# Kernel tuning notes

Hardware: AMD Instinct MI355X
Metric: run time of the kernel (lower is better)

The kernel has to match this reference:

```python
import jax, jax.numpy as jnp
import numpy as np

N, K, D, H = 20000, 32, 256, 8
HD = D // H
DFF = 4 * D
EPS = 1e-5


def _layernorm(x, gamma, beta):
    mu = jnp.mean(x, axis=-1, keepdims=True)
    var = jnp.mean(jnp.square(x - mu), axis=-1, keepdims=True)
    return (x - mu) * jax.lax.rsqrt(var + EPS) * gamma + beta


def setup_inputs() -> dict:
    key = jax.random.key(0)
    ks = jax.random.split(key, 16)
    s = 0.02
    return {
        "x": jax.random.normal(ks[0], (N, D), jnp.float32),
        "attention_samples": jax.random.randint(ks[1], (N, K), 0, N),
        "Wq": jax.random.normal(ks[2], (D, D), jnp.float32) * s,
        "bq": jnp.zeros((D,), jnp.float32),
        "Wk": jax.random.normal(ks[3], (D, D), jnp.float32) * s,
        "bk": jnp.zeros((D,), jnp.float32),
        "Wv": jax.random.normal(ks[4], (D, D), jnp.float32) * s,
        "bv": jnp.zeros((D,), jnp.float32),
        "Wo": jax.random.normal(ks[5], (D, D), jnp.float32) * s,
        "bo": jnp.zeros((D,), jnp.float32),
        "W1": jax.random.normal(ks[6], (D, DFF), jnp.float32) * s,
        "b1": jnp.zeros((DFF,), jnp.float32),
        "W2": jax.random.normal(ks[7], (DFF, D), jnp.float32) * s,
        "b2": jnp.zeros((D,), jnp.float32),
        "g1": jnp.ones((D,), jnp.float32),
        "be1": jnp.zeros((D,), jnp.float32),
        "g2": jnp.ones((D,), jnp.float32),
        "be2": jnp.zeros((D,), jnp.float32),
    }


def reference(x, attention_samples, Wq, bq, Wk, bk, Wv, bv, Wo, bo,
              W1, b1, W2, b2, g1, be1, g2, be2):
    # --- per-node MHA: query = node itself, keys/values = k sampled neighbors ---
    q = (x @ Wq + bq).reshape(N, H, HD)                    # [N,H,hd]
    g = x[attention_samples]                               # [N,K,D] gathered neighbors
    kk = (g @ Wk + bk).reshape(N, K, H, HD)                # [N,K,H,hd]
    vv = (g @ Wv + bv).reshape(N, K, H, HD)
    scale = 1.0 / jnp.sqrt(jnp.asarray(HD, x.dtype))
    scores = jnp.einsum("nhd,nkhd->nhk", q, kk) * scale    # [N,H,K]
    attn = jax.nn.softmax(scores, axis=-1)
    o = jnp.einsum("nhk,nkhd->nhd", attn, vv).reshape(N, D)
    attn_out = o @ Wo + bo                                 # out_proj
    x = _layernorm(x + attn_out, g1, be1)
    # --- FFN ---
    ff = jax.nn.relu(x @ W1 + b1) @ W2 + b2
    x = _layernorm(x + ff, g2, be2)
    return x
```

## Files before the change

### kernel.cpp

```cpp
#include <hip/hip_runtime.h>

#define NN 20000
#define KNEI 32
#define DIM 256
#define NHEAD 8
#define HDIM 32
#define DFFN 1024
#define QKVD 768

typedef __attribute__((ext_vector_type(8))) __bf16 bf16x8;
typedef __attribute__((ext_vector_type(8))) unsigned short u16x8;
typedef __attribute__((ext_vector_type(4))) unsigned short u16x4;
typedef __attribute__((ext_vector_type(4))) float f32x4;
typedef __attribute__((ext_vector_type(2))) float f32x2;

static __device__ __forceinline__ float b2f(unsigned short u) {
    return __builtin_bit_cast(float, (unsigned)u << 16);
}
static __device__ __forceinline__ float blo(unsigned w) {
    return __builtin_bit_cast(float, w << 16);
}
static __device__ __forceinline__ float bhi(unsigned w) {
    return __builtin_bit_cast(float, w & 0xffff0000u);
}
static __device__ __forceinline__ unsigned short f2b(float f) {
    unsigned u = __builtin_bit_cast(unsigned, f);
    return (unsigned short)((u + 0x7fff + ((u >> 16) & 1)) >> 16);
}

static __device__ __forceinline__ unsigned char fp8enc(float v) {
#if defined(__HIP_DEVICE_COMPILE__) && __has_builtin(__builtin_amdgcn_cvt_pk_fp8_f32)
    return (unsigned char)(__builtin_amdgcn_cvt_pk_fp8_f32(v, v, 0u, false) & 0xffu);
#else
    unsigned u = __builtin_bit_cast(unsigned, v);
    unsigned s = u >> 31;
    unsigned a = u & 0x7fffffffu;
    if (a >= 0x43e00000u) return (unsigned char)((s << 7) | 0x7e);
    float af = __builtin_bit_cast(float, a);
    if (af < 0.015625f) {
        unsigned r = (unsigned)(af * 512.0f + 0.5f);
        if (r >= 8u) return (unsigned char)((s << 7) | 0x08);
        return (unsigned char)((s << 7) | r);
    }
    unsigned lsb = (a >> 20) & 1u;
    a += 0x7ffffu + lsb;
    unsigned e = (a >> 23) - 120u;
    unsigned m = (a >> 20) & 7u;
    unsigned code = (e << 3) | m;
    if (code > 0x7eu) code = 0x7eu;
    return (unsigned char)((s << 7) | code);
#endif
}

template<int SEL>
static __device__ __forceinline__ float fp8dec(unsigned word) {
#if defined(__HIP_DEVICE_COMPILE__) && __has_builtin(__builtin_amdgcn_cvt_f32_fp8)
    return __builtin_amdgcn_cvt_f32_fp8(word, SEL);
#else
    unsigned b = (word >> (SEL * 8)) & 0xffu;
    unsigned s = (b >> 7) & 1u;
    unsigned e = (b >> 3) & 0xfu;
    unsigned m = b & 7u;
    float v;
    if (e == 0) v = (float)m * 0.001953125f;
    else        v = __builtin_bit_cast(float, ((e + 120u) << 23) | (m << 20));
    return s ? -v : v;
#endif
}

template<bool HI>
static __device__ __forceinline__ f32x2 fp8pk(unsigned word) {
#if defined(__HIP_DEVICE_COMPILE__) && __has_builtin(__builtin_amdgcn_cvt_pk_f32_fp8)
    return __builtin_amdgcn_cvt_pk_f32_fp8((int)word, HI);
#else
    f32x2 r;
    r.x = fp8dec<HI ? 2 : 0>(word);
    r.y = fp8dec<HI ? 3 : 1>(word);
    return r;
#endif
}

#define GLD16(src, dst)                                                          \
    __builtin_amdgcn_global_load_lds(                                            \
        (const __attribute__((address_space(1))) void*)(const void*)(src),       \
        (__attribute__((address_space(3))) void*)(void*)(dst), 16, 0, 0)

template<int BM, int RELU, int WF32, int WBF16, int SPLIT>
__global__ __launch_bounds__(256) void gemm_mfma(const unsigned short* __restrict__ A,
                                                 const unsigned short* __restrict__ Bt,
                                                 const float* __restrict__ bias,
                                                 float* __restrict__ Cf,
                                                 unsigned short* __restrict__ Cb,
                                                 unsigned char* __restrict__ kvp,
                                                 int M, int N, int K)
{
    constexpr int BN = 128, BK = 32;
    constexpr int MI = BM / 32;
    constexpr int NI = BN / 32;

    __shared__ unsigned short As[BM * BK];
    __shared__ unsigned short Bs[BN * BK];

    const int tid  = threadIdx.x;
    const int wid  = tid >> 6;
    const int lane = tid & 63;
    const int bm = blockIdx.x * BM;
    const int bn = blockIdx.y * BN;
    const int wr = (wid >> 1) * (BM / 2);
    const int wc = (wid & 1) * (BN / 2);
    const int r0   = lane & 15;
    const int kblk = (lane >> 4) * 8;

    f32x4 acc[MI][NI];
    #pragma unroll
    for (int i = 0; i < MI; ++i)
        #pragma unroll
        for (int j = 0; j < NI; ++j)
            acc[i][j] = (f32x4){0.f, 0.f, 0.f, 0.f};

    for (int k0 = 0; k0 < K; k0 += BK) {
        #pragma unroll
        for (int t = 0; t < (BM * 4) / 256; ++t) {
            int c = t * 256 + tid;
            int row = bm + (c >> 2);
            if (row >= M) row = M - 1;
            GLD16(A + (size_t)row * K + k0 + (c & 3) * 8,
                  &As[(t * 256 + wid * 64) * 8]);
        }
        #pragma unroll
        for (int t = 0; t < (BN * 4) / 256; ++t) {
            int c = t * 256 + tid;
            GLD16(Bt + (size_t)(bn + (c >> 2)) * K + k0 + (c & 3) * 8,
                  &Bs[(t * 256 + wid * 64) * 8]);
        }
        __syncthreads();

        bf16x8 af[MI], bfr[NI];
        #pragma unroll
        for (int mi = 0; mi < MI; ++mi)
            af[mi] = __builtin_bit_cast(bf16x8,
                     *(const u16x8*)&As[(wr + mi * 16 + r0) * BK + kblk]);
        #pragma unroll
        for (int ni = 0; ni < NI; ++ni)
            bfr[ni] = __builtin_bit_cast(bf16x8,
                     *(const u16x8*)&Bs[(wc + ni * 16 + r0) * BK + kblk]);
        #pragma unroll
        for (int mi = 0; mi < MI; ++mi)
            #pragma unroll
            for (int ni = 0; ni < NI; ++ni)
                acc[mi][ni] = __builtin_amdgcn_mfma_f32_16x16x32_bf16(
                    af[mi], bfr[ni], acc[mi][ni], 0, 0, 0);
        __syncthreads();
    }

    const int r4 = (lane >> 4) * 4;
    #pragma unroll
    for (int mi = 0; mi < MI; ++mi)
        #pragma unroll
        for (int ni = 0; ni < NI; ++ni) {
            const int col = bn + wc + ni * 16 + r0;
            const float bb = bias[col];
            #pragma unroll
            for (int r = 0; r < 4; ++r) {
                const int row = bm + wr + mi * 16 + r4 + r;
                if (row < M) {
                    float v = acc[mi][ni][r] + bb;
                    if (RELU) v = fmaxf(v, 0.f);
                    if (SPLIT) {
                        if (col < 256) {
                            Cb[(size_t)row * DIM + col] = f2b(v);
                        } else {
                            const int cc  = col - 256;
                            const int isV = cc >> 8;
                            const int hh  = (cc & 255) >> 5;
                            const int dd  = cc & 31;
                            kvp[((size_t)(hh >> 1) * NN + row) * 128
                                + isV * 64 + (hh & 1) * 32 + dd] = fp8enc(v);
                        }
                    } else {
                        if (WF32)  Cf[(size_t)row * N + col] = v;
                        if (WBF16) Cb[(size_t)row * N + col] = f2b(v);
                    }
                }
            }
        }
}

__global__ __launch_bounds__(256) void attn_f8(const unsigned short* __restrict__ q,
                                               const unsigned char* __restrict__ kvp,
                                               const int* __restrict__ samp,
                                               unsigned short* __restrict__ o)
{
    __shared__ int pkbuf[4][128];

    const int bid = blockIdx.x;
    const int hp  = bid & 3;
    const int tid = threadIdx.x;
    const int wid = tid >> 6;
    const int n   = (bid >> 2) * 4 + wid;
    const int lane = tid & 63;
    const int j = lane & 31;
    const int hs = lane >> 5;
    const int h = hp * 2 + hs;

    const int kidx = samp[n * KNEI + j];

    const uint4* qp = (const uint4*)(q + (size_t)n * DIM + h * HDIM);
    const uint4 qa = qp[0], qb = qp[1], qc = qp[2], qd = qp[3];
    const unsigned qw[16] = {qa.x, qa.y, qa.z, qa.w, qb.x, qb.y, qb.z, qb.w,
                             qc.x, qc.y, qc.z, qc.w, qd.x, qd.y, qd.z, qd.w};

    const unsigned char* krow = kvp + ((size_t)hp * NN + kidx) * 128 + hs * 32;
    const uint4 k0 = *(const uint4*)krow;
    const uint4 k1 = *(const uint4*)(krow + 16);
    const unsigned kw[8] = {k0.x, k0.y, k0.z, k0.w, k1.x, k1.y, k1.z, k1.w};

    float s = 0.f;
    #pragma unroll
    for (int i = 0; i < 8; ++i) {
        f32x2 ka = fp8pk<false>(kw[i]);
        f32x2 kb = fp8pk<true>(kw[i]);
        unsigned q0 = qw[2 * i], q1 = qw[2 * i + 1];
        s = fmaf(blo(q0), ka.x, s);
        s = fmaf(bhi(q0), ka.y, s);
        s = fmaf(blo(q1), kb.x, s);
        s = fmaf(bhi(q1), kb.y, s);
    }
    s *= 0.17677669529663687f;

    float m = s;
    #pragma unroll
    for (int sh = 16; sh; sh >>= 1) m = fmaxf(m, __shfl_xor(m, sh));
    float e = __expf(s - m);
    float sum = e;
    #pragma unroll
    for (int sh = 16; sh; sh >>= 1) sum += __shfl_xor(sum, sh);
    const float p = __fdividef(e, sum);

    pkbuf[wid][hs * 64 + j * 2]     = __builtin_bit_cast(int, p);
    pkbuf[wid][hs * 64 + j * 2 + 1] = kidx << 7;

    const int jg = j >> 3, d8 = j & 7;
    const unsigned vconst = (unsigned)((size_t)hp * NN) * 128u + 64u + hs * 32 + d8 * 4;
    float a0 = 0.f, a1 = 0.f, a2 = 0.f, a3 = 0.f;
    #pragma unroll
    for (int jj = 0; jj < 8; ++jj) {
        const int jn = jg * 8 + jj;
        const int2 pk = *(const int2*)&pkbuf[wid][hs * 64 + jn * 2];
        const float pj = __builtin_bit_cast(float, pk.x);
        const unsigned vw = *(const unsigned*)(kvp + vconst + (unsigned)pk.y);
        f32x2 vlo = fp8pk<false>(vw);
        f32x2 vhi = fp8pk<true>(vw);
        a0 = fmaf(pj, vlo.x, a0);
        a1 = fmaf(pj, vlo.y, a1);
        a2 = fmaf(pj, vhi.x, a2);
        a3 = fmaf(pj, vhi.y, a3);
    }
    a0 += __shfl_xor(a0, 8);  a1 += __shfl_xor(a1, 8);
    a2 += __shfl_xor(a2, 8);  a3 += __shfl_xor(a3, 8);
    a0 += __shfl_xor(a0, 16); a1 += __shfl_xor(a1, 16);
    a2 += __shfl_xor(a2, 16); a3 += __shfl_xor(a3, 16);
    if (jg == 0) {
        u16x4 ov = { f2b(a0), f2b(a1), f2b(a2), f2b(a3) };
        *(u16x4*)(o + (size_t)n * DIM + h * HDIM + d8 * 4) = ov;
    }
}

template<int XF32, int WFOUT>
__global__ __launch_bounds__(256) void add_ln(const float* __restrict__ xf,
                                              const unsigned short* __restrict__ xb,
                                              const unsigned short* __restrict__ y,
                                              const float* __restrict__ gamma,
                                              const float* __restrict__ beta,
                                              float* __restrict__ outf,
                                              unsigned short* __restrict__ outb, int M)
{
    const int row = blockIdx.x * 4 + (threadIdx.x >> 6);
    const int lane = threadIdx.x & 63;
    if (row >= M) return;

    float s0, s1, s2, s3;
    if (XF32) {
        const float4 xv = *(const float4*)(xf + (size_t)row * DIM + lane * 4);
        s0 = xv.x; s1 = xv.y; s2 = xv.z; s3 = xv.w;
    } else {
        const u16x4 xv = *(const u16x4*)(xb + (size_t)row * DIM + lane * 4);
        s0 = b2f(xv[0]); s1 = b2f(xv[1]); s2 = b2f(xv[2]); s3 = b2f(xv[3]);
    }
    const u16x4 yv = *(const u16x4*)(y + (size_t)row * DIM + lane * 4);
    s0 += b2f(yv[0]); s1 += b2f(yv[1]); s2 += b2f(yv[2]); s3 += b2f(yv[3]);

    float sum = s0 + s1 + s2 + s3;
    float sq = s0 * s0 + s1 * s1 + s2 * s2 + s3 * s3;
    #pragma unroll
    for (int sh = 32; sh; sh >>= 1) {
        sum += __shfl_xor(sum, sh);
        sq  += __shfl_xor(sq, sh);
    }
    float mean = sum * (1.f / 256.f);
    float var = sq * (1.f / 256.f) - mean * mean;
    float rstd = rsqrtf(var + 1e-5f);

    const float4 gv = *(const float4*)(gamma + lane * 4);
    const float4 bv = *(const float4*)(beta + lane * 4);
    float o0 = (s0 - mean) * rstd * gv.x + bv.x;
    float o1 = (s1 - mean) * rstd * gv.y + bv.y;
    float o2 = (s2 - mean) * rstd * gv.z + bv.z;
    float o3 = (s3 - mean) * rstd * gv.w + bv.w;
    if (WFOUT) {
        float4 ov = { o0, o1, o2, o3 };
        *(float4*)(outf + (size_t)row * DIM + lane * 4) = ov;
    } else {
        u16x4 bb = { f2b(o0), f2b(o1), f2b(o2), f2b(o3) };
        *(u16x4*)(outb + (size_t)row * DIM + lane * 4) = bb;
    }
}

static __device__ __forceinline__ void trans_tile(const float* __restrict__ W,
                                                  unsigned short* __restrict__ T,
                                                  float (*sh)[33],
                                                  int n0, int k0, int N, int K, int tidx)
{
    const int tx = tidx & 31, ty = tidx >> 5;
    #pragma unroll
    for (int i = 0; i < 32; i += 8)
        sh[ty + i][tx] = W[(size_t)(k0 + ty + i) * N + n0 + tx];
    __syncthreads();
    #pragma unroll
    for (int i = 0; i < 32; i += 8)
        T[(size_t)(n0 + ty + i) * K + k0 + tx] = f2b(sh[tx][ty + i]);
}

__global__ __launch_bounds__(256) void prep_all(const float* __restrict__ Wq,
                                                const float* __restrict__ Wk,
                                                const float* __restrict__ Wv,
                                                const float* __restrict__ Wo,
                                                const float* __restrict__ W1,
                                                const float* __restrict__ W2,
                                                const float* __restrict__ bq,
                                                const float* __restrict__ bk,
                                                const float* __restrict__ bv,
                                                const float* __restrict__ x,
                                                unsigned short* __restrict__ WqkvT,
                                                unsigned short* __restrict__ WoT,
                                                unsigned short* __restrict__ W1T,
                                                unsigned short* __restrict__ W2T,
                                                float* __restrict__ bqkv,
                                                unsigned short* __restrict__ xb)
{
    __shared__ float sh[32][33];
    const int bid = blockIdx.x;
    const int tidx = threadIdx.x;

    if (bid < 256) {
        const float* W; unsigned short* T;
        switch (bid >> 6) {
            case 0:  W = Wq; T = WqkvT;           break;
            case 1:  W = Wk; T = WqkvT + 65536;   break;
            case 2:  W = Wv; T = WqkvT + 131072;  break;
            default: W = Wo; T = WoT;             break;
        }
        const int t = bid & 63;
        trans_tile(W, T, sh, (t & 7) * 32, (t >> 3) * 32, DIM, DIM, tidx);
    } else if (bid < 512) {
        const int t = bid - 256;
        trans_tile(W1, W1T, sh, (t & 31) * 32, (t >> 5) * 32, DFFN, DIM, tidx);
    } else if (bid < 768) {
        const int t = bid - 512;
        trans_tile(W2, W2T, sh, (t & 7) * 32, (t >> 3) * 32, DIM, DFFN, tidx);
    } else if (bid == 768) {
        if (tidx < 256) {
            bqkv[tidx]       = bq[tidx];
            bqkv[tidx + 256] = bk[tidx];
            bqkv[tidx + 512] = bv[tidx];
        }
    } else {
        const int i = (bid - 769) * 256 + tidx;
        if (i < NN * DIM / 4) {
            float4 v = ((const float4*)x)[i];
            u16x4 b = { f2b(v.x), f2b(v.y), f2b(v.z), f2b(v.w) };
            ((u16x4*)xb)[i] = b;
        }
    }
}

extern "C" void kernel_launch(void* const* d_in, const int* in_sizes, int n_in,
                              void* d_out, int out_size, void* d_ws, size_t ws_size,
                              hipStream_t stream)
{
    const float* x    = (const float*)d_in[0];
    const int*   samp = (const int*)  d_in[1];
    const float* Wq = (const float*)d_in[2];  const float* bq = (const float*)d_in[3];
    const float* Wk = (const float*)d_in[4];  const float* bk = (const float*)d_in[5];
    const float* Wv = (const float*)d_in[6];  const float* bv = (const float*)d_in[7];
    const float* Wo = (const float*)d_in[8];  const float* bo = (const float*)d_in[9];
    const float* W1 = (const float*)d_in[10]; const float* b1 = (const float*)d_in[11];
    const float* W2 = (const float*)d_in[12]; const float* b2 = (const float*)d_in[13];
    const float* g1 = (const float*)d_in[14]; const float* be1 = (const float*)d_in[15];
    const float* g2 = (const float*)d_in[16]; const float* be2 = (const float*)d_in[17];
    float* out = (float*)d_out;

    char* w = (char*)d_ws;
    const size_t MB = 1u << 20;
    unsigned short* WqkvT = (unsigned short*)(w + 0);
    unsigned short* WoT   = (unsigned short*)(w + 393216);
    unsigned short* W1T   = (unsigned short*)(w + 524288);
    unsigned short* W2T   = (unsigned short*)(w + 1048576);
    float*          bqkv  = (float*)(w + 1572864);
    unsigned short* xb    = (unsigned short*)(w + 2 * MB);
    unsigned short* qb    = (unsigned short*)(w + 13 * MB);
    unsigned char*  kvp   = (unsigned char*) (w + 24 * MB);
    unsigned short* ob    = xb;
    unsigned short* attno = (unsigned short*)(w + 35 * MB);
    unsigned short* x1b   = (unsigned short*)(w + 46 * MB);
    unsigned short* hmid  = (unsigned short*)(w + 57 * MB);
    unsigned short* ffb   = attno;

    const dim3 blk(256);

    prep_all<<<dim3(769 + NN * DIM / 4 / 256), blk, 0, stream>>>(
        Wq, Wk, Wv, Wo, W1, W2, bq, bk, bv, x,
        WqkvT, WoT, W1T, W2T, bqkv, xb);

    gemm_mfma<128, 0, 0, 0, 1><<<dim3(157, 6), blk, 0, stream>>>(
        xb, WqkvT, bqkv, nullptr, qb, kvp, NN, QKVD, DIM);

    attn_f8<<<dim3(NN), blk, 0, stream>>>(qb, kvp, samp, ob);

    gemm_mfma<64, 0, 0, 1, 0><<<dim3(313, 2), blk, 0, stream>>>(
        ob, WoT, bo, nullptr, attno, nullptr, NN, DIM, DIM);
    add_ln<1, 0><<<dim3(NN / 4), blk, 0, stream>>>(x, nullptr, attno, g1, be1,
                                                   nullptr, x1b, NN);

    gemm_mfma<128, 1, 0, 1, 0><<<dim3(157, 8), blk, 0, stream>>>(
        x1b, W1T, b1, nullptr, hmid, nullptr, NN, DFFN, DIM);
    gemm_mfma<64, 0, 0, 1, 0><<<dim3(313, 2), blk, 0, stream>>>(
        hmid, W2T, b2, nullptr, ffb, nullptr, NN, DIM, DFFN);
    add_ln<0, 1><<<dim3(NN / 4), blk, 0, stream>>>(nullptr, x1b, ffb, g2, be2,
                                                   out, nullptr, NN);
}
```

Before: 171.0 us.

## Fuse output projections with residual add and LayerNorm into one GEMM kernel

Adds a gemm_ln kernel in which each block computes a full 32x256 output row tile. It adds bias and residual, reduces row mean and variance across waves through shared memory, and writes the normalized result. This replaces the Wo GEMM plus add_ln and the W2 GEMM plus add_ln pairs, which removes two launches and the bf16 intermediate round-trips. In exchange the new GEMM is simple and unpipelined, with a small BM of 32, one MFMA per B fragment per k-step, a sync every k-step, and uncoalesced scalar epilogue stores. This may make the K=1024 W2 GEMM slower than the tuned gemm_mfma.

Measured after the change: 164.9 us. 3.6% less time.

```diff
diff --git a/kernel.cpp b/kernel.cpp
--- a/kernel.cpp
+++ b/kernel.cpp
@@ -186,6 +186,123 @@
         }
 }
 
+template<int RESF32, int WFOUT>
+__global__ __launch_bounds__(256) void gemm_ln(const unsigned short* __restrict__ A,
+                                               const unsigned short* __restrict__ Bt,
+                                               const float* __restrict__ bias,
+                                               const float* __restrict__ resf,
+                                               const unsigned short* __restrict__ resb,
+                                               const float* __restrict__ gamma,
+                                               const float* __restrict__ beta,
+                                               float* __restrict__ outf,
+                                               unsigned short* __restrict__ outb,
+                                               int M, int K)
+{
+    constexpr int BM = 32, BN = 256, BK = 32;
+    constexpr int NI = BN / 32;
+
+    __shared__ unsigned short As[BM * BK];
+    __shared__ unsigned short Bs[BN * BK];
+    __shared__ float rs[2][BM][2];
+
+    const int tid  = threadIdx.x;
+    const int wid  = tid >> 6;
+    const int lane = tid & 63;
+    const int bm = blockIdx.x * BM;
+    const int wr = (wid >> 1) * 16;
+    const int wc = (wid & 1) * 128;
+    const int r0   = lane & 15;
+    const int kblk = (lane >> 4) * 8;
+
+    f32x4 acc[NI];
+    #pragma unroll
+    for (int j = 0; j < NI; ++j) acc[j] = (f32x4){0.f, 0.f, 0.f, 0.f};
+
+    for (int k0 = 0; k0 < K; k0 += BK) {
+        if (wid < 2) {
+            int c = tid;
+            GLD16(A + (size_t)(bm + (c >> 2)) * K + k0 + (c & 3) * 8,
+                  &As[(wid * 64) * 8]);
+        }
+        #pragma unroll
+        for (int t = 0; t < 4; ++t) {
+            int c = t * 256 + tid;
+            GLD16(Bt + (size_t)(c >> 2) * K + k0 + (c & 3) * 8,
+                  &Bs[(t * 256 + wid * 64) * 8]);
+        }
+        __syncthreads();
+
+        bf16x8 af = __builtin_bit_cast(bf16x8,
+                    *(const u16x8*)&As[(wr + r0) * BK + kblk]);
+        bf16x8 bfr[NI];
+        #pragma unroll
+        for (int ni = 0; ni < NI; ++ni)
+            bfr[ni] = __builtin_bit_cast(bf16x8,
+                      *(const u16x8*)&Bs[(wc + ni * 16 + r0) * BK + kblk]);
+        #pragma unroll
+        for (int ni = 0; ni < NI; ++ni)
+            acc[ni] = __builtin_amdgcn_mfma_f32_16x16x32_bf16(af, bfr[ni], acc[ni], 0, 0, 0);
+        __syncthreads();
+    }
+
+    const int r4 = (lane >> 4) * 4;
+    float v[NI][4];
+    float rsum[4] = {0.f, 0.f, 0.f, 0.f};
+    float rsq[4]  = {0.f, 0.f, 0.f, 0.f};
+    #pragma unroll
+    for (int ni = 0; ni < NI; ++ni) {
+        const int col = wc + ni * 16 + r0;
+        const float bb = bias[col];
+        #pragma unroll
+        for (int r = 0; r < 4; ++r) {
+            const size_t idx = (size_t)(bm + wr + r4 + r) * DIM + col;
+            const float res = RESF32 ? resf[idx] : b2f(resb[idx]);
+            const float val = acc[ni][r] + bb + res;
+            v[ni][r] = val;
+            rsum[r] += val;
+            rsq[r]  += val * val;
+        }
+    }
+    #pragma unroll
+    for (int sh = 1; sh <= 8; sh <<= 1) {
+        #pragma unroll
+        for (int r = 0; r < 4; ++r) {
+            rsum[r] += __shfl_xor(rsum[r], sh);
+            rsq[r]  += __shfl_xor(rsq[r], sh);
+        }
+    }
+    if (r0 == 0) {
+        #pragma unroll
+        for (int r = 0; r < 4; ++r) {
+            rs[wid & 1][wr + r4 + r][0] = rsum[r];
+            rs[wid & 1][wr + r4 + r][1] = rsq[r];
+        }
+    }
+    __syncthreads();
+    float mean_r[4], rstd_r[4];
+    #pragma unroll
+    for (int r = 0; r < 4; ++r) {
+        const int lrow = wr + r4 + r;
+        const float sum = rs[0][lrow][0] + rs[1][lrow][0];
+        const float sq  = rs[0][lrow][1] + rs[1][lrow][1];
+        const float mean = sum * (1.f / 256.f);
+        mean_r[r] = mean;
+        rstd_r[r] = rsqrtf(sq * (1.f / 256.f) - mean * mean + 1e-5f);
+    }
+    #pragma unroll
+    for (int ni = 0; ni < NI; ++ni) {
+        const int col = wc + ni * 16 + r0;
+        const float g = gamma[col], be = beta[col];
+        #pragma unroll
+        for (int r = 0; r < 4; ++r) {
+            const size_t idx = (size_t)(bm + wr + r4 + r) * DIM + col;
+            const float ov = (v[ni][r] - mean_r[r]) * rstd_r[r] * g + be;
+            if (WFOUT) outf[idx] = ov;
+            else       outb[idx] = f2b(ov);
+        }
+    }
+}
+
 __global__ __launch_bounds__(256) void attn_f8(const unsigned short* __restrict__ q,
                                                const unsigned char* __restrict__ kvp,
                                                const int* __restrict__ samp,
@@ -263,56 +380,6 @@
     if (jg == 0) {
         u16x4 ov = { f2b(a0), f2b(a1), f2b(a2), f2b(a3) };
         *(u16x4*)(o + (size_t)n * DIM + h * HDIM + d8 * 4) = ov;
-    }
-}
-
-template<int XF32, int WFOUT>
-__global__ __launch_bounds__(256) void add_ln(const float* __restrict__ xf,
-                                              const unsigned short* __restrict__ xb,
-                                              const unsigned short* __restrict__ y,
-                                              const float* __restrict__ gamma,
-                                              const float* __restrict__ beta,
-                                              float* __restrict__ outf,
-                                              unsigned short* __restrict__ outb, int M)
-{
-    const int row = blockIdx.x * 4 + (threadIdx.x >> 6);
-    const int lane = threadIdx.x & 63;
-    if (row >= M) return;
-
-    float s0, s1, s2, s3;
-    if (XF32) {
-        const float4 xv = *(const float4*)(xf + (size_t)row * DIM + lane * 4);
-        s0 = xv.x; s1 = xv.y; s2 = xv.z; s3 = xv.w;
-    } else {
-        const u16x4 xv = *(const u16x4*)(xb + (size_t)row * DIM + lane * 4);
-        s0 = b2f(xv[0]); s1 = b2f(xv[1]); s2 = b2f(xv[2]); s3 = b2f(xv[3]);
-    }
-    const u16x4 yv = *(const u16x4*)(y + (size_t)row * DIM + lane * 4);
-    s0 += b2f(yv[0]); s1 += b2f(yv[1]); s2 += b2f(yv[2]); s3 += b2f(yv[3]);
-
-    float sum = s0 + s1 + s2 + s3;
-    float sq = s0 * s0 + s1 * s1 + s2 * s2 + s3 * s3;
-    #pragma unroll
-    for (int sh = 32; sh; sh >>= 1) {
-        sum += __shfl_xor(sum, sh);
-        sq  += __shfl_xor(sq, sh);
-    }
-    float mean = sum * (1.f / 256.f);
-    float var = sq * (1.f / 256.f) - mean * mean;
-    float rstd = rsqrtf(var + 1e-5f);
-
-    const float4 gv = *(const float4*)(gamma + lane * 4);
-    const float4 bv = *(const float4*)(beta + lane * 4);
-    float o0 = (s0 - mean) * rstd * gv.x + bv.x;
-    float o1 = (s1 - mean) * rstd * gv.y + bv.y;
-    float o2 = (s2 - mean) * rstd * gv.z + bv.z;
-    float o3 = (s3 - mean) * rstd * gv.w + bv.w;
-    if (WFOUT) {
-        float4 ov = { o0, o1, o2, o3 };
-        *(float4*)(outf + (size_t)row * DIM + lane * 4) = ov;
-    } else {
-        u16x4 bb = { f2b(o0), f2b(o1), f2b(o2), f2b(o3) };
-        *(u16x4*)(outb + (size_t)row * DIM + lane * 4) = bb;
     }
 }
 
@@ -411,10 +478,8 @@
     unsigned short* qb    = (unsigned short*)(w + 13 * MB);
     unsigned char*  kvp   = (unsigned char*) (w + 24 * MB);
     unsigned short* ob    = xb;
-    unsigned short* attno = (unsigned short*)(w + 35 * MB);
     unsigned short* x1b   = (unsigned short*)(w + 46 * MB);
     unsigned short* hmid  = (unsigned short*)(w + 57 * MB);
-    unsigned short* ffb   = attno;
 
     const dim3 blk(256);
 
@@ -427,15 +492,12 @@
 
     attn_f8<<<dim3(NN), blk, 0, stream>>>(qb, kvp, samp, ob);
 
-    gemm_mfma<64, 0, 0, 1, 0><<<dim3(313, 2), blk, 0, stream>>>(
-        ob, WoT, bo, nullptr, attno, nullptr, NN, DIM, DIM);
-    add_ln<1, 0><<<dim3(NN / 4), blk, 0, stream>>>(x, nullptr, attno, g1, be1,
-                                                   nullptr, x1b, NN);
+    gemm_ln<1, 0><<<dim3(NN / 32), blk, 0, stream>>>(
+        ob, WoT, bo, x, nullptr, g1, be1, nullptr, x1b, NN, DIM);
 
     gemm_mfma<128, 1, 0, 1, 0><<<dim3(157, 8), blk, 0, stream>>>(
         x1b, W1T, b1, nullptr, hmid, nullptr, NN, DFFN, DIM);
-    gemm_mfma<64, 0, 0, 1, 0><<<dim3(313, 2), blk, 0, stream>>>(
-        hmid, W2T, b2, nullptr, ffb, nullptr, NN, DIM, DFFN);
-    add_ln<0, 1><<<dim3(NN / 4), blk, 0, stream>>>(nullptr, x1b, ffb, g2, be2,
-                                                   out, nullptr, NN);
-}
+
+    gemm_ln<0, 1><<<dim3(NN / 32), blk, 0, stream>>>(
+        hmid, W2T, b2, nullptr, x1b, g2, be2, out, nullptr, NN, DFFN);
+}
```
